# Optimization experiments

Measured on AMD Instinct MI355X. Metric: run time of the kernel, lower is better.

Reference implementation:

```python
import jax, jax.numpy as jnp
import numpy as np

KERNELS = (7, 9, 11)   # kernel_sizes, dilation=1 each
HEADS_PER = 2          # num_head // len(kernel_sizes)
HEAD_DIM = 32          # dim // num_head
DIM = 192


def _win_idx(L, K):
    # NATTEN non-causal window start: centered, clamped to stay in-bounds.
    starts = jnp.clip(jnp.arange(L) - K // 2, 0, L - K)
    return starts[:, None] + jnp.arange(K)[None, :]  # [L, K]


def _na2d(q, k, v, K):
    # q,k,v: [B, h, H, W, D]; q pre-scaled. Neighborhood attention, kernel KxK.
    B, h, H, W, D = q.shape
    ih = _win_idx(H, K)  # [H, K]
    iw = _win_idx(W, K)  # [W, K]
    kr = k[:, :, ih]     # [B, h, H, Kh, W, D]  rows gathered once
    # loop over the Kw kernel taps (small fixed structural loop)
    attn = jnp.stack(
        [jnp.einsum('bnijd,bnikjd->bnijk', q, kr[:, :, :, :, iw[:, kw], :])
         for kw in range(K)], axis=-1)                 # [B,h,H,W,Kh,Kw]
    attn = jax.nn.softmax(attn.reshape(B, h, H, W, K * K), axis=-1)
    attn = attn.reshape(B, h, H, W, K, K)
    vr = v[:, :, ih]     # [B, h, H, Kh, W, D]
    y = jnp.zeros_like(q)
    for kw in range(K):
        y = y + jnp.einsum('bnijk,bnikjd->bnijd',
                           attn[..., kw], vr[:, :, :, :, iw[:, kw], :])
    return y             # [B, h, H, W, D]


def _forward(x, w_qkv, b_qkv, w_proj, b_proj):
    B, H, W, C = x.shape
    qkv = x @ w_qkv + b_qkv                      # [B,H,W,3*DIM]
    scale = HEAD_DIM ** -0.5
    outs = []
    off = 0
    for K in KERNELS:
        ch = 3 * HEADS_PER * HEAD_DIM            # 192 per scale
        xi = qkv[..., off:off + ch]
        off += ch
        r = xi.reshape(B, H, W, 3, HEADS_PER, HEAD_DIM)
        q = jnp.transpose(r[:, :, :, 0], (0, 3, 1, 2, 4)) * scale
        k = jnp.transpose(r[:, :, :, 1], (0, 3, 1, 2, 4))
        v = jnp.transpose(r[:, :, :, 2], (0, 3, 1, 2, 4))
        y = _na2d(q, k, v, K)                    # [B,h,H,W,D]
        outs.append(jnp.transpose(y, (0, 2, 3, 1, 4)).reshape(B, H, W, HEADS_PER * HEAD_DIM))
    out = jnp.concatenate(outs, axis=-1)         # [B,H,W,DIM]
    return out @ w_proj + b_proj


def setup_inputs() -> dict:
    key = jax.random.key(0)
    ks = jax.random.split(key, 4)
    x = jax.random.normal(ks[0], (4, 96, 96, DIM), jnp.float32)
    w_qkv = jax.random.normal(ks[1], (DIM, 3 * DIM), jnp.float32) * 0.02
    b_qkv = jnp.zeros((3 * DIM,), jnp.float32)
    w_proj = jax.random.normal(ks[2], (DIM, DIM), jnp.float32) * 0.02
    b_proj = jnp.zeros((DIM,), jnp.float32)
    return {'x': x, 'w_qkv': w_qkv, 'b_qkv': b_qkv, 'w_proj': w_proj, 'b_proj': b_proj}


def reference(x, w_qkv, b_qkv, w_proj, b_proj):
    return _forward(x, w_qkv, b_qkv, w_proj, b_proj)
```

## Files before the change

### kernel.cpp

```cpp
#include <hip/hip_runtime.h>
#include <cstddef>

constexpr int B_ = 4, H_ = 96, W_ = 96, C_ = 192, QKVC = 576;
constexpr int NPIX = B_ * H_ * W_;
constexpr float SCALE = 0.17677669529663689f;

typedef __attribute__((ext_vector_type(8))) short bf16x8;
typedef __attribute__((ext_vector_type(4))) float f32x4;
typedef unsigned short ushort_t;

__device__ __forceinline__ unsigned short f2bf(float f) {
    unsigned int u = __builtin_bit_cast(unsigned int, f);
    u += 0x7fffu + ((u >> 16) & 1u);
    return (unsigned short)(u >> 16);
}
__device__ __forceinline__ float bf2f(unsigned short h) {
    unsigned int u = ((unsigned int)h) << 16;
    return __builtin_bit_cast(float, u);
}
__device__ __forceinline__ unsigned int pack2(unsigned short a, unsigned short b) {
    return (unsigned int)a | ((unsigned int)b << 16);
}

__global__ __launch_bounds__(256) void convert_x_kernel(
    const float* __restrict__ x, ushort_t* __restrict__ xh, int n4)
{
    int i = blockIdx.x * 256 + threadIdx.x;
    if (i >= n4) return;
    float4 v = ((const float4*)x)[i];
    uint2 p;
    p.x = pack2(f2bf(v.x), f2bf(v.y));
    p.y = pack2(f2bf(v.z), f2bf(v.w));
    ((uint2*)xh)[i] = p;
}

__global__ __launch_bounds__(256) void convert_w_kernel(
    const float* __restrict__ w_qkv, const float* __restrict__ w_proj,
    ushort_t* __restrict__ wqt, ushort_t* __restrict__ wpt_h,
    ushort_t* __restrict__ wpt_l)
{
    int idx = blockIdx.x * 256 + threadIdx.x;
    if (idx < 576 * 192) {
        int n = idx / 192, k = idx - n * 192;
        wqt[idx] = f2bf(w_qkv[(size_t)k * 576 + n]);
    } else {
        int i2 = idx - 576 * 192;
        if (i2 < 192 * 192) {
            int n = i2 / 192, k = i2 - n * 192;
            float v = w_proj[(size_t)k * 192 + n];
            unsigned short h = f2bf(v);
            wpt_h[i2] = h;
            wpt_l[i2] = f2bf(v - bf2f(h));
        }
    }
}

template<bool BSPLIT, bool OUTBF, bool VT>
__global__ __launch_bounds__(256) void gemm_mfma2_kernel(
    const ushort_t* __restrict__ A,
    const ushort_t* __restrict__ Bt_h, const ushort_t* __restrict__ Bt_l,
    const float* __restrict__ bias, void* __restrict__ Cout,
    ushort_t* __restrict__ vTout, int M, int N, int K)
{
    constexpr int NPB = BSPLIT ? 2 : 1;
    __shared__ __align__(16) ushort_t As[8 * 64 * 8];
    __shared__ __align__(16) ushort_t Bs[NPB][8 * 192 * 8];

    const int tid = threadIdx.x;
    const int lane = tid & 63;
    const int w = tid >> 6;
    const int wm = (w & 1) * 32;
    const int wn = (w >> 1) * 96;
    const int fm = lane & 15;
    const int fq = lane >> 4;

    const int ntiles = N / 192;
    const int m0 = (blockIdx.x / ntiles) * 64;
    const int n0 = (blockIdx.x % ntiles) * 192;

    f32x4 acc[2][6];
    #pragma unroll
    for (int mi = 0; mi < 2; ++mi)
        #pragma unroll
        for (int ni = 0; ni < 6; ++ni)
            acc[mi][ni] = (f32x4){0.f, 0.f, 0.f, 0.f};

    for (int k0 = 0; k0 < K; k0 += 64) {
        __syncthreads();
        #pragma unroll
        for (int it = 0; it < 2; ++it) {
            int idx = it * 256 + tid;
            int m = idx >> 3, kc = idx & 7;
            uint4 v = *(const uint4*)(A + (size_t)(m0 + m) * K + k0 + kc * 8);
            *(uint4*)(&As[0] + (kc * 64 + (m ^ kc)) * 8) = v;
        }
        #pragma unroll
        for (int it = 0; it < 6; ++it) {
            int idx = it * 256 + tid;
            int n = idx >> 3, kc = idx & 7;
            int phys = kc * 192 + (n ^ kc);
            *(uint4*)(&Bs[0][0] + phys * 8) =
                *(const uint4*)(Bt_h + (size_t)(n0 + n) * K + k0 + kc * 8);
            if constexpr (BSPLIT)
                *(uint4*)(&Bs[NPB - 1][0] + phys * 8) =
                    *(const uint4*)(Bt_l + (size_t)(n0 + n) * K + k0 + kc * 8);
        }
        __syncthreads();

        #pragma unroll
        for (int kt2 = 0; kt2 < 2; ++kt2) {
            const int kc = kt2 * 4 + fq;
            bf16x8 ah[2], bh[6];
            #pragma unroll
            for (int mi = 0; mi < 2; ++mi)
                ah[mi] = *(const bf16x8*)(&As[0] + (kc * 64 + ((wm + mi * 16 + fm) ^ kc)) * 8);
            #pragma unroll
            for (int ni = 0; ni < 6; ++ni)
                bh[ni] = *(const bf16x8*)(&Bs[0][0] + (kc * 192 + ((wn + ni * 16 + fm) ^ kc)) * 8);
            #pragma unroll
            for (int mi = 0; mi < 2; ++mi)
                #pragma unroll
                for (int ni = 0; ni < 6; ++ni)
                    acc[mi][ni] = __builtin_amdgcn_mfma_f32_16x16x32_bf16(
                        ah[mi], bh[ni], acc[mi][ni], 0, 0, 0);
            if constexpr (BSPLIT) {
                bf16x8 bl[6];
                #pragma unroll
                for (int ni = 0; ni < 6; ++ni)
                    bl[ni] = *(const bf16x8*)(&Bs[NPB - 1][0] + (kc * 192 + ((wn + ni * 16 + fm) ^ kc)) * 8);
                #pragma unroll
                for (int mi = 0; mi < 2; ++mi)
                    #pragma unroll
                    for (int ni = 0; ni < 6; ++ni)
                        acc[mi][ni] = __builtin_amdgcn_mfma_f32_16x16x32_bf16(
                            ah[mi], bl[ni], acc[mi][ni], 0, 0, 0);
            }
        }
    }

    #pragma unroll
    for (int ni = 0; ni < 6; ++ni) {
        const int lcol = wn + ni * 16 + fm;
        const int col = n0 + lcol;
        const float bv = bias[col];
        const int vl = lcol - 128;
        #pragma unroll
        for (int mi = 0; mi < 2; ++mi) {
            const int rbase = m0 + wm + mi * 16 + fq * 4;
            #pragma unroll
            for (int r = 0; r < 4; ++r) {
                float val = acc[mi][ni][r] + bv;
                if constexpr (OUTBF)
                    ((ushort_t*)Cout)[(size_t)(rbase + r) * N + col] = f2bf(val);
                else
                    ((float*)Cout)[(size_t)(rbase + r) * N + col] = val;
                if constexpr (VT) {
                    if (vl >= 0) {
                        int pix = rbase + r;
                        int bb = pix / 9216;
                        int rem = pix - bb * 9216;
                        int ii = rem / 96;
                        int jj = rem - ii * 96;
                        int hh = vl >> 5, dd = vl & 31;
                        vTout[((size_t)((bb * 96 + ii) * 6) + (n0 / 192) * 2 + hh) * 3072
                              + dd * 96 + jj] = f2bf(val);
                    }
                }
            }
        }
    }
}

__global__ __launch_bounds__(384, 5) void na2d_kernel(
    const ushort_t* __restrict__ qkv, const ushort_t* __restrict__ vT,
    ushort_t* __restrict__ attn)
{
    __shared__ ushort_t Kb[2][96 * 40];
    __shared__ ushort_t Vtb[2][32 * 104];
    __shared__ ushort_t Pb[6][16 * 40];

    int idx = blockIdx.x;
    const int g = idx % 3; idx /= 3;
    const int h = idx & 1; idx >>= 1;
    const int i = idx % 96;
    const int b = idx / 96;

    const int K = 7 + 2 * g, cc = K >> 1;
    int si = i - cc; if (si < 0) si = 0; if (si > H_ - K) si = H_ - K;

    const int tid = threadIdx.x;
    const int w = tid >> 6, lane = tid & 63;
    const int fm = lane & 15, fq = lane >> 4;
    const int pixbase = w * 16;

    int cb = (pixbase - cc) & ~7;
    if (cb < 0) cb = 0; if (cb > 64) cb = 64;
    const int col0 = cb + fm, col1 = cb + 16 + fm;

    int sj[4];
    #pragma unroll
    for (int r = 0; r < 4; ++r) {
        int jj = pixbase + fq * 4 + r - cc;
        if (jj < 0) jj = 0; if (jj > W_ - K) jj = W_ - K;
        sj[r] = jj;
    }

    const size_t rowstride = (size_t)W_ * QKVC;
    const bf16x8 qfrag = *(const bf16x8*)(
        qkv + (size_t)(b * H_ + i) * rowstride + (size_t)(pixbase + fm) * QKVC
        + g * 192 + h * 32 + fq * 8);

    const int scol = tid >> 2, sch = tid & 3;
    const size_t kgoff = (size_t)scol * QKVC + g * 192 + 64 + h * 32 + sch * 8;
    const int klds = scol * 40 + ((sch ^ (scol & 3)) << 3);
    const int vd = tid / 12, vc8 = tid - vd * 12;
    const int vlds = vd * 104 + vc8 * 8;
    const size_t vslice = ((size_t)((b * H_ + si) * 6) + g * 2 + h) * 3072;

    f32x4 y0 = {0.f, 0.f, 0.f, 0.f}, y1 = {0.f, 0.f, 0.f, 0.f};
    float lacc[4] = {0.f, 0.f, 0.f, 0.f};

    uint4 kv = *(const uint4*)(qkv + (size_t)(b * H_ + si) * rowstride + kgoff);
    uint4 vv = *(const uint4*)(vT + vslice + (size_t)tid * 8);

    for (int t = 0; t < K; ++t) {
        *(uint4*)&Kb[t & 1][klds] = kv;
        *(uint4*)&Vtb[t & 1][vlds] = vv;
        if (t + 1 < K) {
            kv = *(const uint4*)(qkv + (size_t)(b * H_ + si + t + 1) * rowstride + kgoff);
            vv = *(const uint4*)(vT + vslice + (size_t)(t + 1) * 18432 + (size_t)tid * 8);
        }
        __syncthreads();

        bf16x8 kf0 = *(const bf16x8*)&Kb[t & 1][col0 * 40 + ((fq ^ (col0 & 3)) << 3)];
        bf16x8 kf1 = *(const bf16x8*)&Kb[t & 1][col1 * 40 + ((fq ^ (col1 & 3)) << 3)];
        f32x4 s0 = __builtin_amdgcn_mfma_f32_16x16x32_bf16(
            qfrag, kf0, (f32x4){0.f, 0.f, 0.f, 0.f}, 0, 0, 0);
        f32x4 s1 = __builtin_amdgcn_mfma_f32_16x16x32_bf16(
            qfrag, kf1, (f32x4){0.f, 0.f, 0.f, 0.f}, 0, 0, 0);

        #pragma unroll
        for (int r = 0; r < 4; ++r) {
            float e0 = __expf(s0[r] * SCALE);
            float e1 = __expf(s1[r] * SCALE);
            e0 = ((unsigned)(col0 - sj[r]) < (unsigned)K) ? e0 : 0.f;
            e1 = ((unsigned)(col1 - sj[r]) < (unsigned)K) ? e1 : 0.f;
            unsigned short p0 = f2bf(e0), p1 = f2bf(e1);
            lacc[r] += bf2f(p0) + bf2f(p1);
            const int m = fq * 4 + r;
            Pb[w][m * 40 + (((fm >> 3) ^ (m & 3)) << 3) + (fm & 7)] = p0;
            Pb[w][m * 40 + ((((fm >> 3) + 2) ^ (m & 3)) << 3) + (fm & 7)] = p1;
        }

        bf16x8 pf = *(const bf16x8*)&Pb[w][fm * 40 + ((fq ^ (fm & 3)) << 3)];
        bf16x8 vf0 = *(const bf16x8*)&Vtb[t & 1][fm * 104 + cb + fq * 8];
        bf16x8 vf1 = *(const bf16x8*)&Vtb[t & 1][(16 + fm) * 104 + cb + fq * 8];
        y0 = __builtin_amdgcn_mfma_f32_16x16x32_bf16(pf, vf0, y0, 0, 0, 0);
        y1 = __builtin_amdgcn_mfma_f32_16x16x32_bf16(pf, vf1, y1, 0, 0, 0);
    }

    #pragma unroll
    for (int r = 0; r < 4; ++r) {
        float l = lacc[r];
        l += __shfl_xor(l, 1); l += __shfl_xor(l, 2);
        l += __shfl_xor(l, 4); l += __shfl_xor(l, 8);
        const float inv = 1.f / l;
        const int j = pixbase + fq * 4 + r;
        const size_t o = (size_t)((b * H_ + i) * W_ + j) * C_ + g * 64 + h * 32 + fm;
        attn[o]      = f2bf(y0[r] * inv);
        attn[o + 16] = f2bf(y1[r] * inv);
    }
}

extern "C" void kernel_launch(void* const* d_in, const int* in_sizes, int n_in,
                              void* d_out, int out_size, void* d_ws, size_t ws_size,
                              hipStream_t stream)
{
    const float* x      = (const float*)d_in[0];
    const float* w_qkv  = (const float*)d_in[1];
    const float* b_qkv  = (const float*)d_in[2];
    const float* w_proj = (const float*)d_in[3];
    const float* b_proj = (const float*)d_in[4];
    float* out = (float*)d_out;

    char* ws = (char*)d_ws;
    ushort_t* qkvh  = (ushort_t*)ws;
    char*     reg1  = ws + (size_t)NPIX * QKVC * 2;
    ushort_t* xh    = (ushort_t*)reg1;
    ushort_t* attn  = (ushort_t*)reg1;
    char*     wbase = reg1 + (size_t)NPIX * C_ * 2;
    ushort_t* wqt   = (ushort_t*)wbase;
    ushort_t* wpt_h = (ushort_t*)(wbase + 576 * 192 * 2);
    ushort_t* wpt_l = (ushort_t*)(wbase + 576 * 192 * 2 + 192 * 192 * 2);
    ushort_t* vT    = (ushort_t*)(wbase + 576 * 192 * 2 + 2 * 192 * 192 * 2);

    convert_x_kernel<<<(NPIX * C_ / 4 + 255) / 256, 256, 0, stream>>>(
        x, xh, NPIX * C_ / 4);
    convert_w_kernel<<<(576 * 192 + 192 * 192 + 255) / 256, 256, 0, stream>>>(
        w_qkv, w_proj, wqt, wpt_h, wpt_l);

    gemm_mfma2_kernel<false, true, true><<<(NPIX / 64) * (QKVC / 192), 256, 0, stream>>>(
        xh, wqt, nullptr, b_qkv, qkvh, vT, NPIX, QKVC, C_);

    na2d_kernel<<<2304, 384, 0, stream>>>(qkvh, vT, attn);

    gemm_mfma2_kernel<true, false, false><<<(NPIX / 64) * (C_ / 192), 256, 0, stream>>>(
        attn, wpt_h, wpt_l, b_proj, out, nullptr, NPIX, C_, C_);
}
```

Measured before the change: 187.8 us.

## Tune GEMM tiles, swizzle block order, use exp2 with additive mask, pack vT stores

Several independent changes land together. The GEMM kernel gains an NT template parameter, and the projection GEMM uses 96-wide N tiles, which doubles its grid. Both the GEMM and na2d kernels remap block IDs with an 8-way interleave to change scheduling locality. In na2d, exp(s*scale) with a select becomes exp2 of an fma with a precomputed additive -1e30 mask. In the QKV GEMM, the V-part stores go out as 64-bit packed transposed writes and no longer also write the regular qkv buffer for V columns, which is safe only if na2d reads V solely from vT.

```diff
diff --git a/kernel.cpp b/kernel.cpp
--- a/kernel.cpp
+++ b/kernel.cpp
@@ -3,7 +3,7 @@
 
 constexpr int B_ = 4, H_ = 96, W_ = 96, C_ = 192, QKVC = 576;
 constexpr int NPIX = B_ * H_ * W_;
-constexpr float SCALE = 0.17677669529663689f;
+constexpr float C2 = 0.25503486208385085f;
 
 typedef __attribute__((ext_vector_type(8))) short bf16x8;
 typedef __attribute__((ext_vector_type(4))) float f32x4;
@@ -20,6 +20,13 @@
 }
 __device__ __forceinline__ unsigned int pack2(unsigned short a, unsigned short b) {
     return (unsigned int)a | ((unsigned int)b << 16);
+}
+__device__ __forceinline__ float fexp2(float x) {
+#if __has_builtin(__builtin_amdgcn_exp2f)
+    return __builtin_amdgcn_exp2f(x);
+#else
+    return __expf(x * 0.6931471805599453f);
+#endif
 }
 
 __global__ __launch_bounds__(256) void convert_x_kernel(
@@ -55,7 +62,7 @@
     }
 }
 
-template<bool BSPLIT, bool OUTBF, bool VT>
+template<bool BSPLIT, bool OUTBF, bool VT, int NT>
 __global__ __launch_bounds__(256) void gemm_mfma2_kernel(
     const ushort_t* __restrict__ A,
     const ushort_t* __restrict__ Bt_h, const ushort_t* __restrict__ Bt_l,
@@ -63,26 +70,29 @@
     ushort_t* __restrict__ vTout, int M, int N, int K)
 {
     constexpr int NPB = BSPLIT ? 2 : 1;
+    constexpr int NI = NT / 32;
     __shared__ __align__(16) ushort_t As[8 * 64 * 8];
-    __shared__ __align__(16) ushort_t Bs[NPB][8 * 192 * 8];
+    __shared__ __align__(16) ushort_t Bs[NPB][8 * NT * 8];
 
     const int tid = threadIdx.x;
     const int lane = tid & 63;
     const int w = tid >> 6;
     const int wm = (w & 1) * 32;
-    const int wn = (w >> 1) * 96;
+    const int wn = (w >> 1) * (NT / 2);
     const int fm = lane & 15;
     const int fq = lane >> 4;
 
-    const int ntiles = N / 192;
-    const int m0 = (blockIdx.x / ntiles) * 64;
-    const int n0 = (blockIdx.x % ntiles) * 192;
-
-    f32x4 acc[2][6];
+    const int phys = blockIdx.x;
+    const int bid = (phys & 7) * (int)(gridDim.x >> 3) + (phys >> 3);
+    const int ntiles = N / NT;
+    const int m0 = (bid / ntiles) * 64;
+    const int n0 = (bid % ntiles) * NT;
+
+    f32x4 acc[2][NI];
     #pragma unroll
     for (int mi = 0; mi < 2; ++mi)
         #pragma unroll
-        for (int ni = 0; ni < 6; ++ni)
+        for (int ni = 0; ni < NI; ++ni)
             acc[mi][ni] = (f32x4){0.f, 0.f, 0.f, 0.f};
 
     for (int k0 = 0; k0 < K; k0 += 64) {
@@ -95,14 +105,14 @@
             *(uint4*)(&As[0] + (kc * 64 + (m ^ kc)) * 8) = v;
         }
         #pragma unroll
-        for (int it = 0; it < 6; ++it) {
+        for (int it = 0; it < NI; ++it) {
             int idx = it * 256 + tid;
             int n = idx >> 3, kc = idx & 7;
-            int phys = kc * 192 + (n ^ kc);
-            *(uint4*)(&Bs[0][0] + phys * 8) =
+            int phys_g = kc * NT + (n ^ kc);
+            *(uint4*)(&Bs[0][0] + phys_g * 8) =
                 *(const uint4*)(Bt_h + (size_t)(n0 + n) * K + k0 + kc * 8);
             if constexpr (BSPLIT)
-                *(uint4*)(&Bs[NPB - 1][0] + phys * 8) =
+                *(uint4*)(&Bs[NPB - 1][0] + phys_g * 8) =
                     *(const uint4*)(Bt_l + (size_t)(n0 + n) * K + k0 + kc * 8);
         }
         __syncthreads();
@@ -110,28 +120,28 @@
         #pragma unroll
         for (int kt2 = 0; kt2 < 2; ++kt2) {
             const int kc = kt2 * 4 + fq;
-            bf16x8 ah[2], bh[6];
+            bf16x8 ah[2], bh[NI];
             #pragma unroll
             for (int mi = 0; mi < 2; ++mi)
                 ah[mi] = *(const bf16x8*)(&As[0] + (kc * 64 + ((wm + mi * 16 + fm) ^ kc)) * 8);
             #pragma unroll
-            for (int ni = 0; ni < 6; ++ni)
-                bh[ni] = *(const bf16x8*)(&Bs[0][0] + (kc * 192 + ((wn + ni * 16 + fm) ^ kc)) * 8);
+            for (int ni = 0; ni < NI; ++ni)
+                bh[ni] = *(const bf16x8*)(&Bs[0][0] + (kc * NT + ((wn + ni * 16 + fm) ^ kc)) * 8);
             #pragma unroll
             for (int mi = 0; mi < 2; ++mi)
                 #pragma unroll
-                for (int ni = 0; ni < 6; ++ni)
+                for (int ni = 0; ni < NI; ++ni)
                     acc[mi][ni] = __builtin_amdgcn_mfma_f32_16x16x32_bf16(
                         ah[mi], bh[ni], acc[mi][ni], 0, 0, 0);
             if constexpr (BSPLIT) {
-                bf16x8 bl[6];
+                bf16x8 bl[NI];
                 #pragma unroll
-                for (int ni = 0; ni < 6; ++ni)
-                    bl[ni] = *(const bf16x8*)(&Bs[NPB - 1][0] + (kc * 192 + ((wn + ni * 16 + fm) ^ kc)) * 8);
+                for (int ni = 0; ni < NI; ++ni)
+                    bl[ni] = *(const bf16x8*)(&Bs[NPB - 1][0] + (kc * NT + ((wn + ni * 16 + fm) ^ kc)) * 8);
                 #pragma unroll
                 for (int mi = 0; mi < 2; ++mi)
                     #pragma unroll
-                    for (int ni = 0; ni < 6; ++ni)
+                    for (int ni = 0; ni < NI; ++ni)
                         acc[mi][ni] = __builtin_amdgcn_mfma_f32_16x16x32_bf16(
                             ah[mi], bl[ni], acc[mi][ni], 0, 0, 0);
             }
@@ -139,7 +149,7 @@
     }
 
     #pragma unroll
-    for (int ni = 0; ni < 6; ++ni) {
+    for (int ni = 0; ni < NI; ++ni) {
         const int lcol = wn + ni * 16 + fm;
         const int col = n0 + lcol;
         const float bv = bias[col];
@@ -147,6 +157,24 @@
         #pragma unroll
         for (int mi = 0; mi < 2; ++mi) {
             const int rbase = m0 + wm + mi * 16 + fq * 4;
+            if constexpr (VT) {
+                if (vl >= 0) {
+                    int bb = rbase / 9216;
+                    int rem = rbase - bb * 9216;
+                    int ii = rem / 96;
+                    int jj = rem - ii * 96;
+                    int hh = vl >> 5, dd = vl & 31;
+                    unsigned long long pk =
+                          (unsigned long long)f2bf(acc[mi][ni][0] + bv)
+                        | ((unsigned long long)f2bf(acc[mi][ni][1] + bv) << 16)
+                        | ((unsigned long long)f2bf(acc[mi][ni][2] + bv) << 32)
+                        | ((unsigned long long)f2bf(acc[mi][ni][3] + bv) << 48);
+                    *(unsigned long long*)(vTout
+                        + ((size_t)((bb * 96 + ii) * 6) + (n0 / 192) * 2 + hh) * 3072
+                        + (size_t)dd * 96 + jj) = pk;
+                    continue;
+                }
+            }
             #pragma unroll
             for (int r = 0; r < 4; ++r) {
                 float val = acc[mi][ni][r] + bv;
@@ -154,18 +182,6 @@
                     ((ushort_t*)Cout)[(size_t)(rbase + r) * N + col] = f2bf(val);
                 else
                     ((float*)Cout)[(size_t)(rbase + r) * N + col] = val;
-                if constexpr (VT) {
-                    if (vl >= 0) {
-                        int pix = rbase + r;
-                        int bb = pix / 9216;
-                        int rem = pix - bb * 9216;
-                        int ii = rem / 96;
-                        int jj = rem - ii * 96;
-                        int hh = vl >> 5, dd = vl & 31;
-                        vTout[((size_t)((bb * 96 + ii) * 6) + (n0 / 192) * 2 + hh) * 3072
-                              + dd * 96 + jj] = f2bf(val);
-                    }
-                }
             }
         }
     }
@@ -179,7 +195,9 @@
     __shared__ ushort_t Vtb[2][32 * 104];
     __shared__ ushort_t Pb[6][16 * 40];
 
-    int idx = blockIdx.x;
+    int phys = blockIdx.x;
+    int idx = (phys & 7) * 288 + (phys >> 3);
+
     const int g = idx % 3; idx /= 3;
     const int h = idx & 1; idx >>= 1;
     const int i = idx % 96;
@@ -197,12 +215,13 @@
     if (cb < 0) cb = 0; if (cb > 64) cb = 64;
     const int col0 = cb + fm, col1 = cb + 16 + fm;
 
-    int sj[4];
+    float bm0[4], bm1[4];
     #pragma unroll
     for (int r = 0; r < 4; ++r) {
         int jj = pixbase + fq * 4 + r - cc;
         if (jj < 0) jj = 0; if (jj > W_ - K) jj = W_ - K;
-        sj[r] = jj;
+        bm0[r] = ((unsigned)(col0 - jj) < (unsigned)K) ? 0.f : -1e30f;
+        bm1[r] = ((unsigned)(col1 - jj) < (unsigned)K) ? 0.f : -1e30f;
     }
 
     const size_t rowstride = (size_t)W_ * QKVC;
@@ -241,10 +260,8 @@
 
         #pragma unroll
         for (int r = 0; r < 4; ++r) {
-            float e0 = __expf(s0[r] * SCALE);
-            float e1 = __expf(s1[r] * SCALE);
-            e0 = ((unsigned)(col0 - sj[r]) < (unsigned)K) ? e0 : 0.f;
-            e1 = ((unsigned)(col1 - sj[r]) < (unsigned)K) ? e1 : 0.f;
+            float e0 = fexp2(fmaf(s0[r], C2, bm0[r]));
+            float e1 = fexp2(fmaf(s1[r], C2, bm1[r]));
             unsigned short p0 = f2bf(e0), p1 = f2bf(e1);
             lacc[r] += bf2f(p0) + bf2f(p1);
             const int m = fq * 4 + r;
@@ -299,11 +316,11 @@
     convert_w_kernel<<<(576 * 192 + 192 * 192 + 255) / 256, 256, 0, stream>>>(
         w_qkv, w_proj, wqt, wpt_h, wpt_l);
 
-    gemm_mfma2_kernel<false, true, true><<<(NPIX / 64) * (QKVC / 192), 256, 0, stream>>>(
+    gemm_mfma2_kernel<false, true, true, 192><<<(NPIX / 64) * (QKVC / 192), 256, 0, stream>>>(
         xh, wqt, nullptr, b_qkv, qkvh, vT, NPIX, QKVC, C_);
 
     na2d_kernel<<<2304, 384, 0, stream>>>(qkvh, vT, attn);
 
-    gemm_mfma2_kernel<true, false, false><<<(NPIX / 64) * (C_ / 192), 256, 0, stream>>>(
+    gemm_mfma2_kernel<true, false, false, 96><<<(NPIX / 64) * (C_ / 96), 256, 0, stream>>>(
         attn, wpt_h, wpt_l, b_proj, out, nullptr, NPIX, C_, C_);
 }
```

After: 161.1 us. 1.17x faster.
